# Performance work log

Measured on AMD Instinct MI355X. Metric: run time of the kernel, lower is better.

## Reference

```python
import jax, jax.numpy as jnp
import numpy as np

HIDDEN = 1024
N_HEADS = 16
HEAD_DIM = HIDDEN // N_HEADS  # 64; RoPE applied only to first HEAD_DIM channels (head 0)
NUM_BUCKETS = 32
MAX_DISTANCE = 128
MLP_HIDDEN = 4 * HIDDEN
B, N = 2, 2048


def _rotate_half(x):
    # interleaved pairs [a0,b0,a1,b1,...] -> [-b0,a0,-b1,a1,...]
    sh = x.shape
    xr = x.reshape(sh[:-1] + (sh[-1] // 2, 2))
    x1, x2 = xr[..., 0], xr[..., 1]
    return jnp.stack([-x2, x1], axis=-1).reshape(sh)


def _rel_bucket(n, num_buckets=NUM_BUCKETS, max_distance=MAX_DISTANCE):
    # bidirectional T5 bucketing
    ctx = jnp.arange(n)[:, None]
    mem = jnp.arange(n)[None, :]
    rp = mem - ctx  # [n, n]
    nb = num_buckets // 2
    buckets = jnp.where(rp > 0, nb, 0)
    rp = jnp.abs(rp)
    max_exact = nb // 2
    is_small = rp < max_exact
    log_ratio = jnp.log(jnp.maximum(rp, 1).astype(jnp.float32) / max_exact)
    rpl = max_exact + (log_ratio / np.log(max_distance / max_exact) * (nb - max_exact)).astype(jnp.int32)
    rpl = jnp.minimum(rpl, nb - 1)
    return buckets + jnp.where(is_small, rp, rpl)


def _ln(x, eps=1e-6):
    # LayerNorm without affine (DiT elementwise_affine=False)
    m = jnp.mean(x, axis=-1, keepdims=True)
    v = jnp.mean(jnp.square(x - m), axis=-1, keepdims=True)
    return (x - m) * jax.lax.rsqrt(v + eps)


def setup_inputs() -> dict:
    key = jax.random.key(0)
    ks = jax.random.split(key, 12)
    s = 0.02
    return {
        "x": jax.random.normal(ks[0], (B, N, HIDDEN), dtype=jnp.float32),
        "c": jax.random.normal(ks[1], (B, HIDDEN), dtype=jnp.float32),
        "w_ada": jax.random.normal(ks[2], (HIDDEN, 6 * HIDDEN), dtype=jnp.float32) * s,
        "b_ada": jnp.zeros((6 * HIDDEN,), dtype=jnp.float32),
        "w_qkv": jax.random.normal(ks[3], (HIDDEN, 3 * HIDDEN), dtype=jnp.float32) * s,
        "b_qkv": jnp.zeros((3 * HIDDEN,), dtype=jnp.float32),
        "w_out": jax.random.normal(ks[4], (HIDDEN, HIDDEN), dtype=jnp.float32) * s,
        "b_out": jnp.zeros((HIDDEN,), dtype=jnp.float32),
        "rel_table": jax.random.normal(ks[5], (NUM_BUCKETS, N_HEADS), dtype=jnp.float32) * s,
        "w_mlp1": jax.random.normal(ks[6], (HIDDEN, MLP_HIDDEN), dtype=jnp.float32) * s,
        "b_mlp1": jnp.zeros((MLP_HIDDEN,), dtype=jnp.float32),
        "w_mlp2": jax.random.normal(ks[7], (MLP_HIDDEN, HIDDEN), dtype=jnp.float32) * s,
        "b_mlp2": jnp.zeros((HIDDEN,), dtype=jnp.float32),
    }


def reference(x, c, w_ada, b_ada, w_qkv, b_qkv, w_out, b_out, rel_table,
              w_mlp1, b_mlp1, w_mlp2, b_mlp2):
    Bb, n, hid = x.shape
    hd = HEAD_DIM

    # AdaLN-Zero modulation params from conditioning
    mod = jax.nn.silu(c) @ w_ada + b_ada  # [B, 6*hid]
    sh_msa, sc_msa, g_msa, sh_mlp, sc_mlp, g_mlp = jnp.split(mod, 6, axis=-1)

    # --- attention branch ---
    h = _ln(x) * (1.0 + sc_msa[:, None, :]) + sh_msa[:, None, :]
    qkv = h @ w_qkv + b_qkv
    q, k, v = jnp.split(qkv, 3, axis=-1)  # each [B, N, hid]

    # partial RoPE: only first head_dim channels (head 0), interleaved-duplicated freqs
    t = jnp.arange(n, dtype=jnp.float32)
    inv_freq = 1.0 / (10000.0 ** (jnp.arange(0, hd, 2, dtype=jnp.float32) / hd))
    fr = t[:, None] * inv_freq[None, :]               # [N, hd/2]
    fr = jnp.stack([fr, fr], axis=-1).reshape(n, hd)  # [N, hd] interleaved dup
    cos, sin = jnp.cos(fr)[None], jnp.sin(fr)[None]

    def partial_rope(a):
        r, u = a[..., :hd], a[..., hd:]
        r = r * cos + _rotate_half(r) * sin
        return jnp.concatenate([r, u], axis=-1)

    q = partial_rope(q)
    k = partial_rope(k)

    qh = q.reshape(Bb, n, N_HEADS, hd)
    kh = k.reshape(Bb, n, N_HEADS, hd)
    vh = v.reshape(Bb, n, N_HEADS, hd)

    scores = jnp.einsum('bqhd,bkhd->bhqk', qh, kh) / np.float32(np.sqrt(hd))
    bias = rel_table[_rel_bucket(n)]                 # [N, N, H]
    scores = scores + jnp.transpose(bias, (2, 0, 1))[None]  # [1,H,N,N]
    attn = jax.nn.softmax(scores, axis=-1)
    ctxv = jnp.einsum('bhqk,bkhd->bqhd', attn, vh).reshape(Bb, n, hid)
    attn_out = ctxv @ w_out + b_out
    x = x + g_msa[:, None, :] * attn_out

    # --- MLP branch ---
    h2 = _ln(x) * (1.0 + sc_mlp[:, None, :]) + sh_mlp[:, None, :]
    m = jax.nn.gelu(h2 @ w_mlp1 + b_mlp1, approximate=True) @ w_mlp2 + b_mlp2
    return x + g_mlp[:, None, :] * m
```

## Files before the change

kernel.cpp:

```cpp
#include <hip/hip_runtime.h>
#include <hip/hip_bf16.h>

#define SEQ 2048

typedef float f32x4 __attribute__((ext_vector_type(4)));
typedef float f32x16 __attribute__((ext_vector_type(16)));
typedef short short8 __attribute__((ext_vector_type(8)));
typedef int int4v __attribute__((ext_vector_type(4)));

static __device__ __forceinline__ unsigned short f2bf(float f) {
  __hip_bfloat16 h = __float2bfloat16(f);
  unsigned short u;
  __builtin_memcpy(&u, &h, 2);
  return u;
}
static __device__ __forceinline__ float bf2f(unsigned short u) {
  __hip_bfloat16 h;
  __builtin_memcpy(&h, &u, 2);
  return __bfloat162float(h);
}
static __device__ __forceinline__ void gload16(const void* g, void* l) {
  __builtin_amdgcn_global_load_lds(
      (const __attribute__((address_space(1))) void*)g,
      (__attribute__((address_space(3))) void*)l, 16, 0, 0);
}
static __device__ __forceinline__ float gelu_t(float x) {
  float t = x * x;
  float z = x * fmaf(0.1029442695044937f, t, 2.3021181827964594f);
  return x * __builtin_amdgcn_rcpf(1.f + exp2f(-z));
}
static __device__ __forceinline__ unsigned int cvtpk(float lo, float hi) {
  unsigned int r;
  asm("v_cvt_pk_bf16_f32 %0, %1, %2" : "=v"(r) : "v"(lo), "v"(hi));
  return r;
}


__global__ void silu_k(const float* __restrict__ c, float* __restrict__ o) {
  int i = blockIdx.x * 256 + threadIdx.x;
  float v = c[i];
  o[i] = v / (1.f + expf(-v));
}

__global__ void mod_part_k(const float* __restrict__ siluc, const float* __restrict__ w_ada,
                           float* __restrict__ part) {
  int gid = blockIdx.x * 256 + threadIdx.x;
  int kc = gid / 12288;
  int idx = gid - kc * 12288;
  int b = idx / 6144;
  int j = idx - b * 6144;
  const float* cp = siluc + b * 1024 + kc * 64;
  const float* wp = w_ada + (size_t)kc * 64 * 6144 + j;
  float acc = 0.f;
#pragma unroll 8
  for (int k = 0; k < 64; ++k) acc += cp[k] * wp[(size_t)k * 6144];
  part[gid] = acc;
}

__global__ void mod_reduce_k(const float* __restrict__ part, const float* __restrict__ b_ada,
                             float* __restrict__ mod) {
  int idx = blockIdx.x * 256 + threadIdx.x;
  int j = idx % 6144;
  float a = b_ada[j];
#pragma unroll
  for (int kc = 0; kc < 16; ++kc) a += part[kc * 12288 + idx];
  mod[idx] = a;
}

#define SOFTMAX_M0 16.0f
__global__ void brp_k(const float* __restrict__ rel_table, float* __restrict__ brp) {
  int idx = blockIdx.x * 256 + threadIdx.x;
  int h = idx >> 12, pos = idx & 4095;
  int rp = pos - 2047;
  int bucket = rp > 0 ? 16 : 0;
  int a = rp < 0 ? -rp : rp;
  int bi;
  if (a < 8) {
    bi = a;
  } else {
    bi = 8 + (int)(logf((float)a / 8.f) / 2.772588722239781f * 8.f);
    if (bi > 15) bi = 15;
  }
  brp[idx] = rel_table[(bucket + bi) * 16 + h] * 1.4426950408889634f - SOFTMAX_M0;
}

__global__ void transpose_cvt(const float* __restrict__ src, unsigned short* __restrict__ dst,
                              int K, int N) {
  __shared__ float tile[32][33];
  int nt = blockIdx.x, kt = blockIdx.y;
  int t = threadIdx.x;
  int col = t & 31, r0 = t >> 5;
#pragma unroll
  for (int i = 0; i < 4; ++i) {
    int r = r0 + i * 8;
    tile[r][col] = src[(size_t)(kt * 32 + r) * N + nt * 32 + col];
  }
  __syncthreads();
#pragma unroll
  for (int i = 0; i < 4; ++i) {
    int r = r0 + i * 8;
    dst[(size_t)(nt * 32 + r) * K + kt * 32 + col] = f2bf(tile[col][r]);
  }
}

__global__ void ln_mod(const float* __restrict__ x, const float* __restrict__ mod,
                       unsigned short* __restrict__ out, int sh_off, int sc_off) {
  int row = blockIdx.x;
  int b = row >> 11;
  int t = threadIdx.x;
  const float4 v = ((const float4*)(x + (size_t)row * 1024))[t];
  float s1 = v.x + v.y + v.z + v.w;
  float s2 = v.x * v.x + v.y * v.y + v.z * v.z + v.w * v.w;
#pragma unroll
  for (int off = 32; off; off >>= 1) {
    s1 += __shfl_xor(s1, off);
    s2 += __shfl_xor(s2, off);
  }
  __shared__ float red[8];
  int w = t >> 6, lane = t & 63;
  if (lane == 0) { red[w] = s1; red[4 + w] = s2; }
  __syncthreads();
  s1 = red[0] + red[1] + red[2] + red[3];
  s2 = red[4] + red[5] + red[6] + red[7];
  float mean = s1 * (1.f / 1024.f);
  float var = s2 * (1.f / 1024.f) - mean * mean;
  float rstd = rsqrtf(var + 1e-6f);
  const float* mb = mod + (size_t)b * 6144;
  int col = t * 4;
  ushort4 o4;
  o4.x = f2bf((v.x - mean) * rstd * (1.f + mb[sc_off + col + 0]) + mb[sh_off + col + 0]);
  o4.y = f2bf((v.y - mean) * rstd * (1.f + mb[sc_off + col + 1]) + mb[sh_off + col + 1]);
  o4.z = f2bf((v.z - mean) * rstd * (1.f + mb[sc_off + col + 2]) + mb[sh_off + col + 2]);
  o4.w = f2bf((v.w - mean) * rstd * (1.f + mb[sc_off + col + 3]) + mb[sh_off + col + 3]);
  *((ushort4*)(out + (size_t)row * 1024 + col)) = o4;
}

__global__ void rope_k(unsigned short* __restrict__ qkv) {
  int t = threadIdx.x;
  int row = blockIdx.x * 4 + (t >> 6);
  int sub = t & 63;
  int which = sub >> 5;
  int i = sub & 31;
  int n = row & (SEQ - 1);
  size_t base = (size_t)row * 3072 + which * 1024 + 2 * i;
  float x0 = bf2f(qkv[base]), x1 = bf2f(qkv[base + 1]);
  float freq = exp2f(-(float)(2 * i) * (13.287712379549449f / 64.f));
  float ang = (float)n * freq;
  float s = sinf(ang), co = cosf(ang);
  qkv[base] = f2bf(x0 * co - x1 * s);
  qkv[base + 1] = f2bf(x1 * co + x0 * s);
}

__global__ void kvpack(const unsigned short* __restrict__ qkv, unsigned short* __restrict__ kpk,
                       unsigned short* __restrict__ vpk) {
  const int kt = blockIdx.x;
  const int bh = blockIdx.y;
  const int b = bh >> 4, h = bh & 15;
  const int t = threadIdx.x;
  const int s = t >> 6, lane = t & 63;
  const int l31 = lane & 31, hi = lane >> 5;
  const size_t outbase = ((size_t)(bh * 64 + kt) * 4 + s) * 512 + lane * 8;
  {
    const unsigned short* src =
        qkv + (size_t)(b * SEQ + kt * 32 + l31) * 3072 + 1024 + h * 64 + s * 16 + hi * 8;
    *(short8*)(kpk + outbase) = *(const short8*)src;
  }
  {
    const int krow = kt * 32 + (s & 1) * 16 + hi * 8;
    const int d = (s >> 1) * 32 + l31;
    const unsigned short* src = qkv + (size_t)(b * SEQ + krow) * 3072 + 2048 + h * 64 + d;
    unsigned short v[8];
#pragma unroll
    for (int j = 0; j < 8; ++j) v[j] = src[(size_t)j * 3072];
    *(short8*)(vpk + outbase) = *(const short8*)v;
  }
}

template <int MODE, int BM, int BN, int PIPE>
__global__ __launch_bounds__(256) void gemm_bt(
    const unsigned short* __restrict__ A, const unsigned short* __restrict__ Bt,
    const float* __restrict__ bias, void* __restrict__ outp, const float* __restrict__ res,
    const float* __restrict__ mod, int goff, int N, int K) {
  constexpr int NBUF = PIPE ? 2 : 1;
  __shared__ __align__(16) unsigned short a_lds[NBUF][BM * 64];
  __shared__ __align__(16) unsigned short b_lds[NBUF][BN * 64];
  constexpr int WM = BM / 2, WN = BN / 2;
  constexpr int MT = WM / 16, NT = WN / 16;
  const int t = threadIdx.x;
  const int lane = t & 63;
  const int l15 = lane & 15, l4 = lane >> 4;
  const int w = t >> 6;
  const int wr = w >> 1, wc = w & 1;
  const int gx = gridDim.x;
  const int nwg = gx * gridDim.y;
  int wg = blockIdx.y * gx + blockIdx.x;
  wg = (wg & 7) * (nwg >> 3) + (wg >> 3);
  const int by = wg / gx, bx = wg - by * gx;
  const int rowA0 = by * BM;
  const int rowB0 = bx * BN;
  const int wub = t & ~63;

  f32x4 acc[MT][NT];
#pragma unroll
  for (int m = 0; m < MT; ++m)
#pragma unroll
    for (int n = 0; n < NT; ++n) acc[m][n] = (f32x4){0.f, 0.f, 0.f, 0.f};

  auto stage = [&](int buf, int kt) {
#pragma unroll
    for (int rnd = 0; rnd < BM / 32; ++rnd) {
      const int idx = rnd * 256 + t;
      const int row = idx >> 3;
      const int cb = ((idx & 7) << 4) ^ ((row & 7) << 4);
      const char* sa = (const char*)(A + (size_t)(rowA0 + row) * K + kt) + cb;
      gload16(sa, (char*)(&a_lds[buf][0]) + (size_t)(rnd * 256 + wub) * 16);
    }
#pragma unroll
    for (int rnd = 0; rnd < BN / 32; ++rnd) {
      const int idx = rnd * 256 + t;
      const int row = idx >> 3;
      const int cb = ((idx & 7) << 4) ^ ((row & 7) << 4);
      const char* sb = (const char*)(Bt + (size_t)(rowB0 + row) * K + kt) + cb;
      gload16(sb, (char*)(&b_lds[buf][0]) + (size_t)(rnd * 256 + wub) * 16);
    }
  };

  auto compute = [&](int buf) {
#pragma unroll
    for (int kb = 0; kb < 2; ++kb) {
      short8 af[MT], bfr[NT];
#pragma unroll
      for (int m = 0; m < MT; ++m) {
        int row = wr * WM + m * 16 + l15;
        int cb = (kb * 64 + l4 * 16) ^ ((row & 7) << 4);
        af[m] = *(const short8*)((const char*)(&a_lds[buf][0]) + row * 128 + cb);
      }
#pragma unroll
      for (int n = 0; n < NT; ++n) {
        int row = wc * WN + n * 16 + l15;
        int cb = (kb * 64 + l4 * 16) ^ ((row & 7) << 4);
        bfr[n] = *(const short8*)((const char*)(&b_lds[buf][0]) + row * 128 + cb);
      }
      __builtin_amdgcn_s_setprio(1);
#pragma unroll
      for (int m = 0; m < MT; ++m)
#pragma unroll
        for (int n = 0; n < NT; ++n)
          acc[m][n] = __builtin_amdgcn_mfma_f32_16x16x32_bf16(af[m], bfr[n], acc[m][n], 0, 0, 0);
      __builtin_amdgcn_s_setprio(0);
    }
  };

  if (PIPE) {
    stage(0, 0);
    __syncthreads();
    int cur = 0;
    for (int kt = 0; kt < K; kt += 64) {
      if (kt + 64 < K) stage(cur ^ 1, kt + 64);
      compute(cur);
      __syncthreads();
      cur ^= 1;
    }
  } else {
    for (int kt = 0; kt < K; kt += 64) {
      stage(0, kt);
      __syncthreads();
      compute(0);
      __syncthreads();
    }
  }

#pragma unroll
  for (int n = 0; n < NT; ++n) {
    const int col = rowB0 + wc * WN + n * 16 + l15;
    const float bv = bias[col];
#pragma unroll
    for (int m = 0; m < MT; ++m) {
      const int row0 = rowA0 + wr * WM + m * 16 + l4 * 4;
#pragma unroll
      for (int r = 0; r < 4; ++r) {
        float v = acc[m][n][r] + bv;
        const size_t o = (size_t)(row0 + r) * N + col;
        if (MODE == 0) {
          ((unsigned short*)outp)[o] = f2bf(v);
        } else if (MODE == 1) {
          ((unsigned short*)outp)[o] = f2bf(gelu_t(v));
        } else {
          float g = mod[(size_t)((row0 + r) >> 11) * 6144 + goff + col];
          ((float*)outp)[o] = res[o] + g * v;
        }
      }
    }
  }
}

__global__ __launch_bounds__(256) void attn_k(const unsigned short* __restrict__ qkv,
                                              const unsigned short* __restrict__ kpk,
                                              const unsigned short* __restrict__ vpk,
                                              const float* __restrict__ brp_all,
                                              unsigned short* __restrict__ op0,
                                              unsigned short* __restrict__ op1,
                                              float* __restrict__ lpart) {
  const int t = threadIdx.x;
  const int w = t >> 6;
  const int lane = t & 63;
  const int l31 = lane & 31;
  const int hi = lane >> 5;
  const int wg = blockIdx.x;
  const int xcd = wg & 7, idx = wg >> 3;
  const int bh = xcd * 4 + (idx >> 5);
  const int rem = idx & 31;
  const int qt = rem >> 1, ks = rem & 1;
  const int b = bh >> 4, h = bh & 15;
  const int qw = qt * 128 + w * 32;
  const float SC = 0.125f * 1.4426950408889634f;
  const float* brp = brp_all + (size_t)h * 4096;

  short8 qfr[4];
  {
    const unsigned short* qrow = qkv + (size_t)(b * SEQ + qw + l31) * 3072 + h * 64 + hi * 8;
#pragma unroll
    for (int kk = 0; kk < 4; ++kk) qfr[kk] = *(const short8*)(qrow + kk * 16);
  }
  const float bfar_pos = brp[4095], bfar_neg = brp[0];
  const float* bql = brp + 2047 + 4 * hi - (qw + l31);

  short8 ones;
#pragma unroll
  for (int i = 0; i < 8; ++i) ones[i] = (short)0x3F80;

  const unsigned short* kp = kpk + ((size_t)(bh * 64 + ks * 16)) * 2048 + lane * 8;
  const unsigned short* vp = vpk + ((size_t)(bh * 64 + ks * 16)) * 2048 + lane * 8;

  short8 kfrA[4], vfrA[4], kfrB[4], vfrB[4];
#pragma unroll
  for (int s = 0; s < 4; ++s) {
    kfrA[s] = *(const short8*)(kp + s * 512);
    vfrA[s] = *(const short8*)(vp + s * 512);
  }
  kp += 2048;
  vp += 2048;

  f32x16 oacc0 = {}, oacc1 = {}, lacc = {};
  int kbase = ks * 512;

#define ATTN_TILE(KF, VF, KFN, VFN)                                                       \
  do {                                                                                    \
    KFN[0] = *(const short8*)(kp);                                                        \
    KFN[1] = *(const short8*)(kp + 512);                                                  \
    KFN[2] = *(const short8*)(kp + 1024);                                                 \
    KFN[3] = *(const short8*)(kp + 1536);                                                 \
    VFN[0] = *(const short8*)(vp);                                                        \
    VFN[1] = *(const short8*)(vp + 512);                                                  \
    VFN[2] = *(const short8*)(vp + 1024);                                                 \
    VFN[3] = *(const short8*)(vp + 1536);                                                 \
    kp += 2048;                                                                           \
    vp += 2048;                                                                           \
    f32x16 sacc = {};                                                                     \
    sacc = __builtin_amdgcn_mfma_f32_32x32x16_bf16(KF[0], qfr[0], sacc, 0, 0, 0);         \
    sacc = __builtin_amdgcn_mfma_f32_32x32x16_bf16(KF[1], qfr[1], sacc, 0, 0, 0);         \
    sacc = __builtin_amdgcn_mfma_f32_32x32x16_bf16(KF[2], qfr[2], sacc, 0, 0, 0);         \
    sacc = __builtin_amdgcn_mfma_f32_32x32x16_bf16(KF[3], qfr[3], sacc, 0, 0, 0);         \
    float p[16];                                                                          \
    const int dd = kbase - qw;                                                            \
    if (dd >= 128 || dd <= -128) {                                                        \
      const float bf_ = (dd > 0) ? bfar_pos : bfar_neg;                                   \
      _Pragma("unroll") for (int r = 0; r < 16; ++r)                                      \
          p[r] = __builtin_amdgcn_exp2f(fmaf(sacc[r], SC, bf_));                          \
    } else {                                                                              \
      const float* bp = bql + kbase;                                                      \
      _Pragma("unroll") for (int r = 0; r < 16; ++r)                                      \
          p[r] = __builtin_amdgcn_exp2f(fmaf(sacc[r], SC, bp[(r & 3) + 8 * (r >> 2)]));   \
    }                                                                                     \
    unsigned int x0 = cvtpk(p[0], p[1]), x1 = cvtpk(p[2], p[3]);                          \
    unsigned int y0 = cvtpk(p[4], p[5]), y1 = cvtpk(p[6], p[7]);                          \
    asm("v_permlane32_swap_b32 %0, %1" : "+v"(x0), "+v"(y0));                             \
    asm("v_permlane32_swap_b32 %0, %1" : "+v"(x1), "+v"(y1));                             \
    unsigned int x2 = cvtpk(p[8], p[9]), x3 = cvtpk(p[10], p[11]);                        \
    unsigned int y2 = cvtpk(p[12], p[13]), y3 = cvtpk(p[14], p[15]);                      \
    asm("v_permlane32_swap_b32 %0, %1" : "+v"(x2), "+v"(y2));                             \
    asm("v_permlane32_swap_b32 %0, %1" : "+v"(x3), "+v"(y3));                             \
    int4v pi0 = {(int)x0, (int)x1, (int)y0, (int)y1};                                     \
    int4v pi1 = {(int)x2, (int)x3, (int)y2, (int)y3};                                     \
    short8 pf0 = __builtin_bit_cast(short8, pi0);                                         \
    short8 pf1 = __builtin_bit_cast(short8, pi1);                                         \
    lacc = __builtin_amdgcn_mfma_f32_32x32x16_bf16(ones, pf0, lacc, 0, 0, 0);             \
    lacc = __builtin_amdgcn_mfma_f32_32x32x16_bf16(ones, pf1, lacc, 0, 0, 0);             \
    oacc0 = __builtin_amdgcn_mfma_f32_32x32x16_bf16(VF[0], pf0, oacc0, 0, 0, 0);          \
    oacc0 = __builtin_amdgcn_mfma_f32_32x32x16_bf16(VF[1], pf1, oacc0, 0, 0, 0);          \
    oacc1 = __builtin_amdgcn_mfma_f32_32x32x16_bf16(VF[2], pf0, oacc1, 0, 0, 0);          \
    oacc1 = __builtin_amdgcn_mfma_f32_32x32x16_bf16(VF[3], pf1, oacc1, 0, 0, 0);          \
    kbase += 32;                                                                          \
  } while (0)

#pragma unroll 1
  for (int it = 0; it < 8; ++it) {
    ATTN_TILE(kfrA, vfrA, kfrB, vfrB);
    ATTN_TILE(kfrB, vfrB, kfrA, vfrA);
  }
#undef ATTN_TILE

  unsigned short* op = ks ? op1 : op0;
  unsigned short* orow = op + (size_t)(b * SEQ + qw + l31) * 1024 + h * 64;
#pragma unroll
  for (int r = 0; r < 16; r += 2) {
    const int d = (r & 3) + 8 * (r >> 2) + 4 * hi;
    *(unsigned int*)(orow + d) = cvtpk(oacc0[r], oacc0[r + 1]);
    *(unsigned int*)(orow + 32 + d) = cvtpk(oacc1[r], oacc1[r + 1]);
  }
  if (lane < 32) lpart[(size_t)ks * 65536 + (size_t)(b * SEQ + qw + l31) * 16 + h] = lacc[0];
}

__global__ void attn_combine(const unsigned short* __restrict__ op0,
                             const unsigned short* __restrict__ op1,
                             const float* __restrict__ lpart,
                             unsigned short* __restrict__ ctxv) {
  const int row = blockIdx.x;
  const int t = threadIdx.x;
  const int h = t >> 4;
  const size_t base = (size_t)row * 1024 + t * 4;
  ushort4 a = *(const ushort4*)(op0 + base);
  ushort4 c = *(const ushort4*)(op1 + base);
  const float l = lpart[(size_t)row * 16 + h] + lpart[65536 + (size_t)row * 16 + h];
  const float inv = 1.f / l;
  ushort4 o;
  o.x = f2bf((bf2f(a.x) + bf2f(c.x)) * inv);
  o.y = f2bf((bf2f(a.y) + bf2f(c.y)) * inv);
  o.z = f2bf((bf2f(a.z) + bf2f(c.z)) * inv);
  o.w = f2bf((bf2f(a.w) + bf2f(c.w)) * inv);
  *(ushort4*)(ctxv + base) = o;
}

extern "C" void kernel_launch(void* const* d_in, const int* in_sizes, int n_in, void* d_out,
                              int out_size, void* d_ws, size_t ws_size, hipStream_t stream) {
  (void)in_sizes; (void)n_in; (void)out_size; (void)ws_size;
  const float* x = (const float*)d_in[0];
  const float* c = (const float*)d_in[1];
  const float* w_ada = (const float*)d_in[2];
  const float* b_ada = (const float*)d_in[3];
  const float* w_qkv = (const float*)d_in[4];
  const float* b_qkv = (const float*)d_in[5];
  const float* w_out = (const float*)d_in[6];
  const float* b_out = (const float*)d_in[7];
  const float* rel_t = (const float*)d_in[8];
  const float* w_mlp1 = (const float*)d_in[9];
  const float* b_mlp1 = (const float*)d_in[10];
  const float* w_mlp2 = (const float*)d_in[11];
  const float* b_mlp2 = (const float*)d_in[12];
  float* out = (float*)d_out;
  char* ws = (char*)d_ws;

  constexpr size_t OFF_WQKVT = 0;
  constexpr size_t OFF_WOUTT = OFF_WQKVT + (size_t)3072 * 1024 * 2;
  constexpr size_t OFF_WM1T = OFF_WOUTT + (size_t)1024 * 1024 * 2;
  constexpr size_t OFF_WM2T = OFF_WM1T + (size_t)4096 * 1024 * 2;
  constexpr size_t OFF_H = OFF_WM2T + (size_t)1024 * 4096 * 2;
  constexpr size_t OFF_QKV = OFF_H + (size_t)4096 * 1024 * 2;
  constexpr size_t OFF_VT = OFF_QKV + (size_t)4096 * 3072 * 2;
  constexpr size_t OFF_CTXV = OFF_VT + (size_t)32 * 64 * 2048 * 2;
  constexpr size_t OFF_MID = OFF_CTXV + (size_t)4096 * 1024 * 2;
  constexpr size_t OFF_SILU = OFF_MID + (size_t)4096 * 4096 * 2;
  constexpr size_t OFF_MOD = OFF_SILU + 2048 * 4;
  constexpr size_t OFF_BRP = OFF_MOD + 12288 * 4;
  constexpr size_t OFF_PART = OFF_BRP + 65536 * 4;
  constexpr size_t OFF_OPART0 = OFF_H;
  constexpr size_t OFF_OPART1 = OFF_MID + (size_t)16 * 1024 * 1024;
  constexpr size_t OFF_LPART = OFF_PART;

  unsigned short* wqkvT = (unsigned short*)(ws + OFF_WQKVT);
  unsigned short* woutT = (unsigned short*)(ws + OFF_WOUTT);
  unsigned short* wm1T = (unsigned short*)(ws + OFF_WM1T);
  unsigned short* wm2T = (unsigned short*)(ws + OFF_WM2T);
  unsigned short* hbuf = (unsigned short*)(ws + OFF_H);
  unsigned short* qkvbuf = (unsigned short*)(ws + OFF_QKV);
  unsigned short* vpkbuf = (unsigned short*)(ws + OFF_VT);
  unsigned short* ctxvbuf = (unsigned short*)(ws + OFF_CTXV);
  unsigned short* midbuf = (unsigned short*)(ws + OFF_MID);
  unsigned short* kpkbuf = (unsigned short*)(ws + OFF_MID);
  float* siluc = (float*)(ws + OFF_SILU);
  float* modb = (float*)(ws + OFF_MOD);
  float* brp = (float*)(ws + OFF_BRP);
  float* part = (float*)(ws + OFF_PART);
  unsigned short* op0 = (unsigned short*)(ws + OFF_OPART0);
  unsigned short* op1 = (unsigned short*)(ws + OFF_OPART1);
  float* lpart = (float*)(ws + OFF_LPART);

  silu_k<<<8, 256, 0, stream>>>(c, siluc);
  mod_part_k<<<768, 256, 0, stream>>>(siluc, w_ada, part);
  mod_reduce_k<<<48, 256, 0, stream>>>(part, b_ada, modb);
  transpose_cvt<<<dim3(96, 32), 256, 0, stream>>>(w_qkv, wqkvT, 1024, 3072);
  transpose_cvt<<<dim3(32, 32), 256, 0, stream>>>(w_out, woutT, 1024, 1024);
  transpose_cvt<<<dim3(128, 32), 256, 0, stream>>>(w_mlp1, wm1T, 1024, 4096);
  transpose_cvt<<<dim3(32, 128), 256, 0, stream>>>(w_mlp2, wm2T, 4096, 1024);
  brp_k<<<256, 256, 0, stream>>>(rel_t, brp);

  ln_mod<<<4096, 256, 0, stream>>>(x, modb, hbuf, 0, 1024);
  gemm_bt<0, 128, 128, 0><<<dim3(24, 32), 256, 0, stream>>>(hbuf, wqkvT, b_qkv, qkvbuf, nullptr,
                                                            nullptr, 0, 3072, 1024);
  rope_k<<<1024, 256, 0, stream>>>(qkvbuf);
  kvpack<<<dim3(64, 32), 256, 0, stream>>>(qkvbuf, kpkbuf, vpkbuf);
  attn_k<<<1024, 256, 0, stream>>>(qkvbuf, kpkbuf, vpkbuf, brp, op0, op1, lpart);
  attn_combine<<<4096, 256, 0, stream>>>(op0, op1, lpart, ctxvbuf);
  gemm_bt<2, 64, 64, 1><<<dim3(16, 64), 256, 0, stream>>>(ctxvbuf, woutT, b_out, out, x, modb,
                                                          2048, 1024, 1024);
  ln_mod<<<4096, 256, 0, stream>>>(out, modb, hbuf, 3072, 4096);
  gemm_bt<1, 128, 128, 0><<<dim3(32, 32), 256, 0, stream>>>(hbuf, wm1T, b_mlp1, midbuf, nullptr,
                                                            nullptr, 0, 4096, 1024);
  gemm_bt<2, 64, 64, 1><<<dim3(16, 64), 256, 0, stream>>>(midbuf, wm2T, b_mlp2, out, out, modb,
                                                          5120, 1024, 4096);
}
```

Before: 251.7 us.

## Fuse RoPE into kvpack and attention; merge small prep and transpose launches

Removes the standalone RoPE kernel. Keys for head 0 are rotated while kvpack repacks them, and queries for head 0 are rotated after they are loaded into registers in the attention kernel. SiLU and relative-bias table prep are merged into one launch, and the four weight transposes into a single launch. The aim is fewer kernel launches and one less read-modify-write pass over the QKV buffer, at the cost of a branch on h==0 and extra transcendental math in the attention prologue.

```diff
diff --git a/kernel.cpp b/kernel.cpp
--- a/kernel.cpp
+++ b/kernel.cpp
@@ -34,12 +34,40 @@
   asm("v_cvt_pk_bf16_f32 %0, %1, %2" : "=v"(r) : "v"(lo), "v"(hi));
   return r;
 }
-
-
-__global__ void silu_k(const float* __restrict__ c, float* __restrict__ o) {
-  int i = blockIdx.x * 256 + threadIdx.x;
-  float v = c[i];
-  o[i] = v / (1.f + expf(-v));
+static __device__ __forceinline__ void rope_pair(short8& v, int m, int i, float pos) {
+  const float fr = exp2f(-(float)(2 * i) * (13.287712379549449f / 64.f));
+  const float ang = pos * fr;
+  const float sn = sinf(ang), cs = cosf(ang);
+  const float x0 = bf2f((unsigned short)v[2 * m]);
+  const float x1 = bf2f((unsigned short)v[2 * m + 1]);
+  v[2 * m] = (short)f2bf(x0 * cs - x1 * sn);
+  v[2 * m + 1] = (short)f2bf(x1 * cs + x0 * sn);
+}
+
+
+#define SOFTMAX_M0 16.0f
+__global__ void prep_misc(const float* __restrict__ c, float* __restrict__ siluc,
+                          const float* __restrict__ rel_table, float* __restrict__ brp) {
+  const int bid = blockIdx.x, t = threadIdx.x;
+  if (bid < 8) {
+    int i = bid * 256 + t;
+    float v = c[i];
+    siluc[i] = v / (1.f + expf(-v));
+  } else {
+    int idx = (bid - 8) * 256 + t;
+    int h = idx >> 12, pos = idx & 4095;
+    int rp = pos - 2047;
+    int bucket = rp > 0 ? 16 : 0;
+    int a = rp < 0 ? -rp : rp;
+    int bi;
+    if (a < 8) {
+      bi = a;
+    } else {
+      bi = 8 + (int)(logf((float)a / 8.f) / 2.772588722239781f * 8.f);
+      if (bi > 15) bi = 15;
+    }
+    brp[idx] = rel_table[(bucket + bi) * 16 + h] * 1.4426950408889634f - SOFTMAX_M0;
+  }
 }
 
 __global__ void mod_part_k(const float* __restrict__ siluc, const float* __restrict__ w_ada,
@@ -67,39 +95,37 @@
   mod[idx] = a;
 }
 
-#define SOFTMAX_M0 16.0f
-__global__ void brp_k(const float* __restrict__ rel_table, float* __restrict__ brp) {
-  int idx = blockIdx.x * 256 + threadIdx.x;
-  int h = idx >> 12, pos = idx & 4095;
-  int rp = pos - 2047;
-  int bucket = rp > 0 ? 16 : 0;
-  int a = rp < 0 ? -rp : rp;
-  int bi;
-  if (a < 8) {
-    bi = a;
+__global__ void transpose_all(const float* __restrict__ w_qkv, const float* __restrict__ w_out,
+                              const float* __restrict__ w_mlp1, const float* __restrict__ w_mlp2,
+                              unsigned short* __restrict__ dq, unsigned short* __restrict__ dwo,
+                              unsigned short* __restrict__ dm1, unsigned short* __restrict__ dm2) {
+  __shared__ float tile[32][33];
+  const int bid = blockIdx.x;
+  const float* src;
+  unsigned short* dst;
+  int K, N, NT, r;
+  if (bid < 3072) {
+    src = w_qkv; dst = dq; K = 1024; N = 3072; NT = 96; r = bid;
+  } else if (bid < 4096) {
+    src = w_out; dst = dwo; K = 1024; N = 1024; NT = 32; r = bid - 3072;
+  } else if (bid < 8192) {
+    src = w_mlp1; dst = dm1; K = 1024; N = 4096; NT = 128; r = bid - 4096;
   } else {
-    bi = 8 + (int)(logf((float)a / 8.f) / 2.772588722239781f * 8.f);
-    if (bi > 15) bi = 15;
-  }
-  brp[idx] = rel_table[(bucket + bi) * 16 + h] * 1.4426950408889634f - SOFTMAX_M0;
-}
-
-__global__ void transpose_cvt(const float* __restrict__ src, unsigned short* __restrict__ dst,
-                              int K, int N) {
-  __shared__ float tile[32][33];
-  int nt = blockIdx.x, kt = blockIdx.y;
-  int t = threadIdx.x;
-  int col = t & 31, r0 = t >> 5;
+    src = w_mlp2; dst = dm2; K = 4096; N = 1024; NT = 32; r = bid - 8192;
+  }
+  const int nt = r % NT, kt = r / NT;
+  const int t = threadIdx.x;
+  const int col = t & 31, r0 = t >> 5;
 #pragma unroll
   for (int i = 0; i < 4; ++i) {
-    int r = r0 + i * 8;
-    tile[r][col] = src[(size_t)(kt * 32 + r) * N + nt * 32 + col];
+    int rr = r0 + i * 8;
+    tile[rr][col] = src[(size_t)(kt * 32 + rr) * N + nt * 32 + col];
   }
   __syncthreads();
 #pragma unroll
   for (int i = 0; i < 4; ++i) {
-    int r = r0 + i * 8;
-    dst[(size_t)(nt * 32 + r) * K + kt * 32 + col] = f2bf(tile[col][r]);
+    int rr = r0 + i * 8;
+    dst[(size_t)(nt * 32 + rr) * K + kt * 32 + col] = f2bf(tile[col][rr]);
   }
 }
 
@@ -135,22 +161,6 @@
   *((ushort4*)(out + (size_t)row * 1024 + col)) = o4;
 }
 
-__global__ void rope_k(unsigned short* __restrict__ qkv) {
-  int t = threadIdx.x;
-  int row = blockIdx.x * 4 + (t >> 6);
-  int sub = t & 63;
-  int which = sub >> 5;
-  int i = sub & 31;
-  int n = row & (SEQ - 1);
-  size_t base = (size_t)row * 3072 + which * 1024 + 2 * i;
-  float x0 = bf2f(qkv[base]), x1 = bf2f(qkv[base + 1]);
-  float freq = exp2f(-(float)(2 * i) * (13.287712379549449f / 64.f));
-  float ang = (float)n * freq;
-  float s = sinf(ang), co = cosf(ang);
-  qkv[base] = f2bf(x0 * co - x1 * s);
-  qkv[base + 1] = f2bf(x1 * co + x0 * s);
-}
-
 __global__ void kvpack(const unsigned short* __restrict__ qkv, unsigned short* __restrict__ kpk,
                        unsigned short* __restrict__ vpk) {
   const int kt = blockIdx.x;
@@ -163,7 +173,14 @@
   {
     const unsigned short* src =
         qkv + (size_t)(b * SEQ + kt * 32 + l31) * 3072 + 1024 + h * 64 + s * 16 + hi * 8;
-    *(short8*)(kpk + outbase) = *(const short8*)src;
+    short8 kv = *(const short8*)src;
+    if (h == 0) {
+      const float pos = (float)(kt * 32 + l31);
+      const int d0 = s * 16 + hi * 8;
+#pragma unroll
+      for (int m = 0; m < 4; ++m) rope_pair(kv, m, (d0 >> 1) + m, pos);
+    }
+    *(short8*)(kpk + outbase) = kv;
   }
   {
     const int krow = kt * 32 + (s & 1) * 16 + hi * 8;
@@ -321,6 +338,15 @@
     const unsigned short* qrow = qkv + (size_t)(b * SEQ + qw + l31) * 3072 + h * 64 + hi * 8;
 #pragma unroll
     for (int kk = 0; kk < 4; ++kk) qfr[kk] = *(const short8*)(qrow + kk * 16);
+    if (h == 0) {
+      const float pos = (float)(qw + l31);
+#pragma unroll
+      for (int kk = 0; kk < 4; ++kk) {
+        const int d0 = kk * 16 + hi * 8;
+#pragma unroll
+        for (int m = 0; m < 4; ++m) rope_pair(qfr[kk], m, (d0 >> 1) + m, pos);
+      }
+    }
   }
   const float bfar_pos = brp[4095], bfar_neg = brp[0];
   const float* bql = brp + 2047 + 4 * hi - (qw + l31);
@@ -485,19 +511,15 @@
   unsigned short* op1 = (unsigned short*)(ws + OFF_OPART1);
   float* lpart = (float*)(ws + OFF_LPART);
 
-  silu_k<<<8, 256, 0, stream>>>(c, siluc);
+  prep_misc<<<264, 256, 0, stream>>>(c, siluc, rel_t, brp);
   mod_part_k<<<768, 256, 0, stream>>>(siluc, w_ada, part);
   mod_reduce_k<<<48, 256, 0, stream>>>(part, b_ada, modb);
-  transpose_cvt<<<dim3(96, 32), 256, 0, stream>>>(w_qkv, wqkvT, 1024, 3072);
-  transpose_cvt<<<dim3(32, 32), 256, 0, stream>>>(w_out, woutT, 1024, 1024);
-  transpose_cvt<<<dim3(128, 32), 256, 0, stream>>>(w_mlp1, wm1T, 1024, 4096);
-  transpose_cvt<<<dim3(32, 128), 256, 0, stream>>>(w_mlp2, wm2T, 4096, 1024);
-  brp_k<<<256, 256, 0, stream>>>(rel_t, brp);
+  transpose_all<<<12288, 256, 0, stream>>>(w_qkv, w_out, w_mlp1, w_mlp2, wqkvT, woutT, wm1T,
+                                           wm2T);
 
   ln_mod<<<4096, 256, 0, stream>>>(x, modb, hbuf, 0, 1024);
   gemm_bt<0, 128, 128, 0><<<dim3(24, 32), 256, 0, stream>>>(hbuf, wqkvT, b_qkv, qkvbuf, nullptr,
                                                             nullptr, 0, 3072, 1024);
-  rope_k<<<1024, 256, 0, stream>>>(qkvbuf);
   kvpack<<<dim3(64, 32), 256, 0, stream>>>(qkvbuf, kpkbuf, vpkbuf);
   attn_k<<<1024, 256, 0, stream>>>(qkvbuf, kpkbuf, vpkbuf, brp, op0, op1, lpart);
   attn_combine<<<4096, 256, 0, stream>>>(op0, op1, lpart, ctxvbuf);
```

New measurement: 242.8 us. 3.6% less time.
